# Performance work log

Hardware: AMD Instinct MI355X
Metric: run time of the kernel (lower is better)

The kernel has to match this reference:

```python
import jax, jax.numpy as jnp
import numpy as np

N_S = 4096      # number of sentences
N_K = 8192      # number of knowledge entries
HID = 1024      # settings.hidden_dim
SENT = 1024     # settings.sent_dim


def setup_inputs() -> dict:
    key = jax.random.key(0)
    ks = jax.random.split(key, 6)
    sentences = jax.random.normal(ks[0], (N_S, SENT), dtype=jnp.float32)
    knowledge = jax.random.normal(ks[1], (N_K, 3 * HID), dtype=jnp.float32)
    # Linear params stored as [in, out] for x @ W + b
    Ws = jax.random.normal(ks[2], (SENT, HID), dtype=jnp.float32) * 0.02
    bs = jnp.zeros((HID,), dtype=jnp.float32)
    Wk = jax.random.normal(ks[3], (3 * HID, HID), dtype=jnp.float32) * 0.02
    bk = jnp.zeros((HID,), dtype=jnp.float32)
    return {"sentences": sentences, "knowledge": knowledge,
            "Ws": Ws, "bs": bs, "Wk": Wk, "bk": bk}


def reference(sentences, knowledge, Ws, bs, Wk, bk):
    S = sentences @ Ws + bs                  # [N_s, h]
    K = knowledge @ Wk + bk                  # [N_k, h]
    align_scores = S @ K.T                   # [N_s, N_k]
    # NOTE: softmax over dim=0 (sentence axis), exactly as the torch module
    attentions = jax.nn.softmax(align_scores, axis=0)
    fused = attentions @ knowledge           # [N_s, 3h]
    return (fused, attentions)
```

## Files before the change

### kernel.cpp

```cpp
#include <hip/hip_runtime.h>
#include <hip/hip_bf16.h>
#include <cstdint>
#include <cstddef>

#define N_S 4096
#define N_Kn 8192
#define HID 1024
#define SENT 1024
#define K3 3072

typedef __attribute__((ext_vector_type(4))) float f4;
typedef __attribute__((ext_vector_type(8))) short bf8;
typedef __attribute__((ext_vector_type(4))) short bf4;
typedef unsigned short u16;

__device__ __forceinline__ u16 f2bf(float x) {
    __hip_bfloat16 h = __float2bfloat16(x);
    return __builtin_bit_cast(u16, h);
}
__device__ __forceinline__ float bf2f(u16 u) {
    union { unsigned int u; float f; } v; v.u = ((unsigned int)u) << 16;
    return v.f;
}

__device__ __forceinline__ void gl16(const u16* g, u16* l) {
    __builtin_amdgcn_global_load_lds(
        (const __attribute__((address_space(1))) void*)g,
        (__attribute__((address_space(3))) void*)l, 16, 0, 0);
}

__device__ __forceinline__ int xcd_swz(int bid, int nwg) {
    const int cpx = nwg >> 3;
    return (bid & 7) * cpx + (bid >> 3);
}

#define BARR __builtin_amdgcn_s_barrier()
#define PRIO1 __builtin_amdgcn_s_setprio(1)
#define PRIO0 __builtin_amdgcn_s_setprio(0)
#define VM7  asm volatile("s_waitcnt vmcnt(7)" ::: "memory")
#define VM6  asm volatile("s_waitcnt vmcnt(6)" ::: "memory")
#define VM0  asm volatile("s_waitcnt vmcnt(0)" ::: "memory")

__global__ __launch_bounds__(256) void transpose_split_f32(
    const float* __restrict__ in, u16* __restrict__ hi, u16* __restrict__ lo,
    int R, int C)
{
    __shared__ float tile[32][33];
    const int bx = blockIdx.x * 32, by = blockIdx.y * 32;
    const int tx = threadIdx.x & 31, ty = threadIdx.x >> 5;
#pragma unroll
    for (int i = 0; i < 32; i += 8)
        tile[ty + i][tx] = in[(size_t)(by + ty + i) * C + bx + tx];
    __syncthreads();
#pragma unroll
    for (int i = 0; i < 32; i += 8) {
        const float v = tile[tx][ty + i];
        const u16 h = f2bf(v);
        const size_t o = (size_t)(bx + ty + i) * R + by + tx;
        hi[o] = h;
        lo[o] = f2bf(v - bf2f(h));
    }
}

__global__ __launch_bounds__(256) void transpose_f32_bf16(
    const float* __restrict__ in, u16* __restrict__ out, int R, int C)
{
    __shared__ float tile[32][33];
    const int bx = blockIdx.x * 32, by = blockIdx.y * 32;
    const int tx = threadIdx.x & 31, ty = threadIdx.x >> 5;
#pragma unroll
    for (int i = 0; i < 32; i += 8)
        tile[ty + i][tx] = in[(size_t)(by + ty + i) * C + bx + tx];
    __syncthreads();
#pragma unroll
    for (int i = 0; i < 32; i += 8)
        out[(size_t)(bx + ty + i) * R + by + tx] = f2bf(tile[tx][ty + i]);
}

#define GB_LDA(buf, mh) \
  _Pragma("unroll") for (int mf_ = 0; mf_ < 2; ++mf_) \
  _Pragma("unroll") for (int kk_ = 0; kk_ < 2; ++kk_) \
    fa[mf_][kk_] = *(const bf8*)&sA[buf][(wm*64 + ((mh)*2+mf_)*16 + fr)*64 + (((kk_*4+kg) ^ (fr&7))<<3)];

#define GB_LDB(buf, nh, FB) \
  _Pragma("unroll") for (int nf_ = 0; nf_ < 3; ++nf_) \
  _Pragma("unroll") for (int kk_ = 0; kk_ < 2; ++kk_) \
    FB[nf_][kk_] = *(const bf8*)&sB[buf][(wn*96 + ((nh)*3+nf_)*16 + fr)*64 + (((kk_*4+kg) ^ (fr&7))<<3)];

#define GB_MMA(mh, nh, FB) \
  _Pragma("unroll") for (int kk_ = 0; kk_ < 2; ++kk_) \
  _Pragma("unroll") for (int mf_ = 0; mf_ < 2; ++mf_) \
  _Pragma("unroll") for (int nf_ = 0; nf_ < 3; ++nf_) \
    acc[(mh)*2+mf_][(nh)*3+nf_] = __builtin_amdgcn_mfma_f32_16x16x32_bf16( \
        fa[mf_][kk_], FB[nf_][kk_], acc[(mh)*2+mf_][(nh)*3+nf_], 0, 0, 0);

__global__ __launch_bounds__(512, 2) void gemm8b(
    const u16* __restrict__ A, const u16* __restrict__ B,
    float* __restrict__ C, int N, int Kd, int gx)
{
    __shared__ u16 sA[2][256 * 64];
    __shared__ u16 sB[2][192 * 64];

    const int swz = xcd_swz(blockIdx.x, gridDim.x);
    const int bx = swz % gx, by = swz / gx;
    const long brow = (long)by * 256, bcol = (long)bx * 192;

    const int t = threadIdx.x;
    const int w = t >> 6, l = t & 63;
    const int fr = l & 15, kg = l >> 4;
    const int wm = w >> 1;
    const int wn = w & 1;

    const int srow = t >> 3;
    const int schk = ((t & 7) ^ (srow & 7)) << 3;
    const int sldb = w << 9;

    const u16* pA0 = A + (brow +   0 + srow) * (long)Kd + schk;
    const u16* pA1 = A + (brow +  64 + srow) * (long)Kd + schk;
    const u16* pA2 = A + (brow + 128 + srow) * (long)Kd + schk;
    const u16* pA3 = A + (brow + 192 + srow) * (long)Kd + schk;
    const u16* pB0 = B + (bcol +   0 + srow) * (long)Kd + schk;
    const u16* pB1 = B + (bcol +  64 + srow) * (long)Kd + schk;
    const u16* pB2 = B + (bcol + 128 + srow) * (long)Kd + schk;

    auto stB3 = [&](int buf) {
        u16* base = &sB[buf][0];
        gl16(pB0, base + sldb);
        gl16(pB1, base + 4096 + sldb);
        gl16(pB2, base + 8192 + sldb);
    };
    auto stA4 = [&](int buf) {
        u16* base = &sA[buf][0];
        gl16(pA0, base + sldb);
        gl16(pA1, base + 4096 + sldb);
        gl16(pA2, base + 8192 + sldb);
        gl16(pA3, base + 12288 + sldb);
    };
    auto advance = [&]() {
        pA0 += 64; pA1 += 64; pA2 += 64; pA3 += 64;
        pB0 += 64; pB1 += 64; pB2 += 64;
    };

    f4 acc[4][6];
#pragma unroll
    for (int m = 0; m < 4; ++m)
#pragma unroll
        for (int n = 0; n < 6; ++n) acc[m][n] = (f4){0.f, 0.f, 0.f, 0.f};

    bf8 fa[2][2], fb0[3][2], fb1[3][2];

    const int NK = Kd >> 6;

    stB3(0); stA4(0); advance();
    stB3(1); stA4(1); advance();
    VM7;
    BARR;
    GB_LDB(0, 0, fb0);

    for (int kt = 0; kt < NK; ++kt) {
        const int buf = kt & 1;
        const bool s2 = kt + 2 < NK;
        const bool more = kt + 1 < NK;

        GB_LDA(buf, 0);
        BARR; PRIO1; GB_MMA(0, 0, fb0); PRIO0;

        GB_LDB(buf, 1, fb1);
        BARR; PRIO1; GB_MMA(0, 1, fb1); PRIO0;

        GB_LDA(buf, 1);
        if (s2) { stB3(buf); }
        BARR; PRIO1; GB_MMA(1, 0, fb0); PRIO0;

        if (s2) { stA4(buf); VM7; } else { VM0; }
        BARR;
        if (more) { GB_LDB(buf ^ 1, 0, fb0); }
        PRIO1; GB_MMA(1, 1, fb1); PRIO0;
        advance();
    }

#pragma unroll
    for (int n = 0; n < 6; ++n) {
        const long c = bcol + wn * 96 + n * 16 + fr;
#pragma unroll
        for (int m = 0; m < 4; ++m) {
            const long r0 = brow + wm * 64 + m * 16 + kg * 4;
#pragma unroll
            for (int r = 0; r < 4; ++r)
                C[(r0 + r) * (long)N + c] = acc[m][n][r];
        }
    }
}

#define GS_LD(buf) \
  _Pragma("unroll") for (int m_ = 0; m_ < 4; ++m_) { \
    fah[m_] = *(const bf8*)&sAh[buf][(wm*64 + m_*16 + fr)*32 + kq]; \
    fal[m_] = *(const bf8*)&sAl[buf][(wm*64 + m_*16 + fr)*32 + kq]; } \
  _Pragma("unroll") for (int j_ = 0; j_ < 4; ++j_) { \
    fbh[j_] = *(const bf8*)&sBh[buf][(wn*64 + j_*16 + fr)*32 + kq]; \
    fbl[j_] = *(const bf8*)&sBl[buf][(wn*64 + j_*16 + fr)*32 + kq]; }

#define GS_MMA(nlo) \
  _Pragma("unroll") for (int m_ = 0; m_ < 4; ++m_) \
  _Pragma("unroll") for (int j_ = 0; j_ < 2; ++j_) { \
    const int n_ = (nlo)*2 + j_; \
    acc[m_][n_] = __builtin_amdgcn_mfma_f32_16x16x32_bf16(fah[m_], fbh[n_], acc[m_][n_], 0, 0, 0); \
    acc[m_][n_] = __builtin_amdgcn_mfma_f32_16x16x32_bf16(fah[m_], fbl[n_], acc[m_][n_], 0, 0, 0); \
    acc[m_][n_] = __builtin_amdgcn_mfma_f32_16x16x32_bf16(fal[m_], fbh[n_], acc[m_][n_], 0, 0, 0); }

__global__ __launch_bounds__(512, 2) void gemm8s(
    const u16* __restrict__ Ah, const u16* __restrict__ Al,
    const u16* __restrict__ Bh, const u16* __restrict__ Bl,
    float* __restrict__ C, int N, int Kd)
{
    __shared__ u16 sAh[2][8192], sAl[2][8192];
    __shared__ u16 sBh[2][4096], sBl[2][4096];

    const int bid = blockIdx.x;
    const int q = bid >> 3;
    const int by = (bid & 7) * 2 + (q & 1);
    const int bx = q >> 1;
    const long brow = (long)by * 256, bcol = (long)bx * 128;

    const int t = threadIdx.x;
    const int w = t >> 6, l = t & 63;
    const int fr = l & 15, kg = l >> 4;
    const int wm = w >> 1;
    const int wn = w & 1;
    const int kq = (kg ^ ((fr >> 1) & 3)) << 3;

    const int srow = t >> 2;
    const int schk = ((t & 3) ^ ((t >> 3) & 3)) << 3;
    const int sldb = w << 9;

    const u16* pAh0 = Ah + (brow + srow) * (long)Kd + schk;
    const u16* pAh1 = Ah + (brow + 128 + srow) * (long)Kd + schk;
    const u16* pAl0 = Al + (brow + srow) * (long)Kd + schk;
    const u16* pAl1 = Al + (brow + 128 + srow) * (long)Kd + schk;
    const u16* pBh0 = Bh + (bcol + srow) * (long)Kd + schk;
    const u16* pBl0 = Bl + (bcol + srow) * (long)Kd + schk;

    auto stage6 = [&](int buf) {
        gl16(pBh0, &sBh[buf][sldb]);
        gl16(pBl0, &sBl[buf][sldb]);
        gl16(pAh0, &sAh[buf][sldb]);
        gl16(pAh1, &sAh[buf][4096 + sldb]);
        gl16(pAl0, &sAl[buf][sldb]);
        gl16(pAl1, &sAl[buf][4096 + sldb]);
    };
    auto advance = [&]() {
        pAh0 += 32; pAh1 += 32; pAl0 += 32; pAl1 += 32;
        pBh0 += 32; pBl0 += 32;
    };

    f4 acc[4][4];
#pragma unroll
    for (int m = 0; m < 4; ++m)
#pragma unroll
        for (int n = 0; n < 4; ++n) acc[m][n] = (f4){0.f, 0.f, 0.f, 0.f};

    bf8 fah[4], fal[4], fbh[4], fbl[4];

    const int NK = Kd >> 5;

    stage6(0); advance();
    stage6(1); advance();
    VM6;
    BARR;

    for (int kt = 0; kt < NK; ++kt) {
        const int buf = kt & 1;
        const bool s2 = kt + 2 < NK;

        GS_LD(buf);
        BARR; PRIO1; GS_MMA(0); PRIO0;

        if (s2) { stage6(buf); VM6; } else { VM0; }
        BARR;
        PRIO1; GS_MMA(1); PRIO0;
        advance();
    }

#pragma unroll
    for (int n = 0; n < 4; ++n) {
        const long c = bcol + wn * 64 + n * 16 + fr;
#pragma unroll
        for (int m = 0; m < 4; ++m) {
            const long r0 = brow + wm * 64 + m * 16 + kg * 4;
#pragma unroll
            for (int r = 0; r < 4; ++r)
                C[(r0 + r) * (long)N + c] = acc[m][n][r];
        }
    }
}

template <bool SPLIT, bool AF32, bool EPIS>
__global__ __launch_bounds__(256) void gemm_mfma(
    const void* __restrict__ Aany, const u16* __restrict__ Alo_,
    const u16* __restrict__ Bhi_, const u16* __restrict__ Blo_,
    float* __restrict__ Cf, u16* __restrict__ Chi, u16* __restrict__ Clo,
    const float* __restrict__ bias, int N, int Kd, int gx)
{
    constexpr int SA = AF32 ? 48 : 32;
    __shared__ u16 sAh[128 * SA];
    __shared__ u16 sAl[SPLIT ? 128 * SA : 8];
    __shared__ u16 sBh[128 * 32];
    __shared__ u16 sBl[SPLIT ? 128 * 32 : 8];

    const int swz = xcd_swz(blockIdx.x, gridDim.x);
    const int nst_x = gx >> 2;
    const int st = swz >> 4, off = swz & 15;
    const int bxi = (st % nst_x) * 4 + (off & 3);
    const int byi = (st / nst_x) * 4 + (off >> 2);

    const int t = threadIdx.x;
    const int w = t >> 6;
    const int l = t & 63;
    const long brow = (long)byi * 128;
    const long bcol = (long)bxi * 128;

    const int grow = l >> 2;
    const int gcol = ((l & 3) ^ ((l >> 3) & 3)) * 8;

    const int wr = (w >> 1) * 64;
    const int wc = (w & 1) * 64;
    const int fr = l & 15;
    const int kg = l >> 4;
    const int kq = (kg ^ ((fr >> 1) & 3)) * 8;

    f4 acc[4][4];
#pragma unroll
    for (int m = 0; m < 4; m++)
#pragma unroll
        for (int n = 0; n < 4; n++) acc[m][n] = (f4){0.f, 0.f, 0.f, 0.f};

    const int nkt = Kd >> 5;
    for (int kt = 0; kt < nkt; ++kt) {
        const int k0 = kt * 32;

#pragma unroll
        for (int i = 0; i < 2; ++i) {
            const long r = bcol + i * 64 + w * 16 + grow;
            const int lb = i * 2048 + w * 512;
            gl16(Bhi_ + r * Kd + k0 + gcol, sBh + lb);
            if constexpr (SPLIT) gl16(Blo_ + r * Kd + k0 + gcol, sBl + lb);
        }

        if constexpr (!AF32) {
            const u16* Ahi = (const u16*)Aany;
#pragma unroll
            for (int i = 0; i < 2; ++i) {
                const long r = brow + i * 64 + w * 16 + grow;
                const int lb = i * 2048 + w * 512;
                gl16(Ahi + r * Kd + k0 + gcol, sAh + lb);
                if constexpr (SPLIT) gl16(Alo_ + r * Kd + k0 + gcol, sAl + lb);
            }
        } else {
            const float* Af = (const float*)Aany;
            const int ar = w * 8 + (l >> 3);
            const int cF = (l & 7) * 4;
#pragma unroll
            for (int j = 0; j < 4; ++j) {
                const int r = j * 32 + ar;
                const f4 v = *(const f4*)(Af + (brow + r) * (long)Kd + k0 + cF);
                u16 h[4], lw[4];
#pragma unroll
                for (int q = 0; q < 4; ++q) {
                    h[q] = f2bf(v[q]);
                    if constexpr (SPLIT) lw[q] = f2bf(v[q] - bf2f(h[q]));
                }
                *(bf4*)&sAh[r * SA + cF] = *(bf4*)h;
                if constexpr (SPLIT) *(bf4*)&sAl[r * SA + cF] = *(bf4*)lw;
            }
        }
        __syncthreads();

        bf8 fah[4], fbh[4], fal[4], fbl[4];
#pragma unroll
        for (int m = 0; m < 4; ++m) {
            if constexpr (AF32) {
                fah[m] = *(bf8*)&sAh[(wr + m * 16 + fr) * SA + kg * 8];
                if constexpr (SPLIT) fal[m] = *(bf8*)&sAl[(wr + m * 16 + fr) * SA + kg * 8];
            } else {
                fah[m] = *(bf8*)&sAh[(wr + m * 16 + fr) * 32 + kq];
                if constexpr (SPLIT) fal[m] = *(bf8*)&sAl[(wr + m * 16 + fr) * 32 + kq];
            }
            fbh[m] = *(bf8*)&sBh[(wc + m * 16 + fr) * 32 + kq];
            if constexpr (SPLIT) fbl[m] = *(bf8*)&sBl[(wc + m * 16 + fr) * 32 + kq];
        }
#pragma unroll
        for (int m = 0; m < 4; ++m)
#pragma unroll
            for (int n = 0; n < 4; ++n) {
                acc[m][n] = __builtin_amdgcn_mfma_f32_16x16x32_bf16(fah[m], fbh[n], acc[m][n], 0, 0, 0);
                if constexpr (SPLIT) {
                    acc[m][n] = __builtin_amdgcn_mfma_f32_16x16x32_bf16(fah[m], fbl[n], acc[m][n], 0, 0, 0);
                    acc[m][n] = __builtin_amdgcn_mfma_f32_16x16x32_bf16(fal[m], fbh[n], acc[m][n], 0, 0, 0);
                }
            }
        __syncthreads();
    }

#pragma unroll
    for (int n = 0; n < 4; ++n) {
        const long c = bcol + wc + n * 16 + fr;
        float bv = 0.f;
        if constexpr (EPIS) bv = bias[c];
#pragma unroll
        for (int m = 0; m < 4; ++m) {
            const long r0 = brow + wr + m * 16 + kg * 4;
#pragma unroll
            for (int r = 0; r < 4; ++r) {
                const float v = acc[m][n][r] + bv;
                if constexpr (EPIS) {
                    const u16 h = f2bf(v);
                    Chi[(r0 + r) * (long)N + c] = h;
                    Clo[(r0 + r) * (long)N + c] = f2bf(v - bf2f(h));
                } else {
                    Cf[(r0 + r) * (long)N + c] = v;
                }
            }
        }
    }
}

#define RCHUNK 128

__global__ __launch_bounds__(256) void softmax_partial(
    const float* __restrict__ align, float* __restrict__ pm, float* __restrict__ ps)
{
    const int col = blockIdx.x * 256 + threadIdx.x;
    const int r0 = blockIdx.y * RCHUNK;
    float m = -3.4e38f;
    for (int r = 0; r < RCHUNK; r++)
        m = fmaxf(m, align[(size_t)(r0 + r) * N_Kn + col]);
    float s = 0.f;
    for (int r = 0; r < RCHUNK; r++)
        s += __expf(align[(size_t)(r0 + r) * N_Kn + col] - m);
    pm[(size_t)blockIdx.y * N_Kn + col] = m;
    ps[(size_t)blockIdx.y * N_Kn + col] = s;
}

__global__ __launch_bounds__(256) void softmax_combine(
    const float* __restrict__ pm, const float* __restrict__ ps,
    float* __restrict__ fm, float* __restrict__ fsinv)
{
    const int col = blockIdx.x * 256 + threadIdx.x;
    float m = -3.4e38f;
#pragma unroll
    for (int i = 0; i < 32; i++) m = fmaxf(m, pm[(size_t)i * N_Kn + col]);
    float s = 0.f;
#pragma unroll
    for (int i = 0; i < 32; i++)
        s += ps[(size_t)i * N_Kn + col] * __expf(pm[(size_t)i * N_Kn + col] - m);
    fm[col] = m;
    fsinv[col] = 1.f / s;
}

__global__ __launch_bounds__(256) void softmax_norm(
    float* __restrict__ align, u16* __restrict__ abf,
    const float* __restrict__ fm, const float* __restrict__ fsinv)
{
    const int col = blockIdx.x * 256 + threadIdx.x;
    const int r0 = blockIdx.y * RCHUNK;
    const float m = fm[col], si = fsinv[col];
    for (int r = 0; r < RCHUNK; r++) {
        const size_t idx = (size_t)(r0 + r) * N_Kn + col;
        const float v = __expf(align[idx] - m) * si;
        align[idx] = v;
        abf[idx] = f2bf(v);
    }
}

extern "C" void kernel_launch(void* const* d_in, const int* in_sizes, int n_in,
                              void* d_out, int out_size, void* d_ws, size_t ws_size,
                              hipStream_t stream)
{
    const float* sentences = (const float*)d_in[0];
    const float* knowledge = (const float*)d_in[1];
    const float* Ws = (const float*)d_in[2];
    const float* bs = (const float*)d_in[3];
    const float* Wk = (const float*)d_in[4];
    const float* bk = (const float*)d_in[5];

    float* out_fused = (float*)d_out;
    float* out_attn = (float*)d_out + (size_t)N_S * K3;

    char* w = (char*)d_ws;
    u16* attn_bf = (u16*)w;
    u16* WsT_hi = (u16*)w; w += (size_t)HID * SENT * 2;
    u16* WsT_lo = (u16*)w; w += (size_t)HID * SENT * 2;
    u16* WkT_hi = (u16*)w; w += (size_t)HID * K3 * 2;
    u16* WkT_lo = (u16*)w; w += (size_t)HID * K3 * 2;
    u16* S_hi   = (u16*)w; w += (size_t)N_S * HID * 2;
    u16* S_lo   = (u16*)w; w += (size_t)N_S * HID * 2;
    u16* K_hi   = (u16*)w; w += (size_t)N_Kn * HID * 2;
    u16* K_lo   = (u16*)w; w += (size_t)N_Kn * HID * 2;
    u16* kT     = (u16*)w; w += (size_t)K3 * N_Kn * 2;
    float* pm   = (float*)w; w += (size_t)32 * N_Kn * 4;
    float* ps   = (float*)w; w += (size_t)32 * N_Kn * 4;
    float* fm   = (float*)w; w += (size_t)N_Kn * 4;
    float* fsv  = (float*)w; w += (size_t)N_Kn * 4;

    transpose_split_f32<<<dim3(HID / 32, SENT / 32), 256, 0, stream>>>(Ws, WsT_hi, WsT_lo, SENT, HID);
    transpose_split_f32<<<dim3(HID / 32, K3 / 32), 256, 0, stream>>>(Wk, WkT_hi, WkT_lo, K3, HID);
    transpose_f32_bf16<<<dim3(K3 / 32, N_Kn / 32), 256, 0, stream>>>(knowledge, kT, N_Kn, K3);

    gemm_mfma<true, true, true><<<(HID / 128) * (N_S / 128), 256, 0, stream>>>(
        sentences, nullptr, WsT_hi, WsT_lo, nullptr, S_hi, S_lo, bs, HID, SENT, HID / 128);

    gemm_mfma<true, true, true><<<(HID / 128) * (N_Kn / 128), 256, 0, stream>>>(
        knowledge, nullptr, WkT_hi, WkT_lo, nullptr, K_hi, K_lo, bk, HID, K3, HID / 128);

    gemm8s<<<(N_Kn / 128) * (N_S / 256), 512, 0, stream>>>(
        S_hi, S_lo, K_hi, K_lo, out_attn, N_Kn, HID);

    softmax_partial<<<dim3(N_Kn / 256, N_S / RCHUNK), 256, 0, stream>>>(out_attn, pm, ps);
    softmax_combine<<<dim3(N_Kn / 256), 256, 0, stream>>>(pm, ps, fm, fsv);
    softmax_norm<<<dim3(N_Kn / 256, N_S / RCHUNK), 256, 0, stream>>>(out_attn, attn_bf, fm, fsv);

    gemm8b<<<(K3 / 192) * (N_S / 256), 512, 0, stream>>>(
        attn_bf, kT, out_fused, K3, N_Kn, K3 / 192);
}
```

Baseline: 753.2 us.

## Fuse column softmax partial max/sum into attention GEMM epilogue

Computes per-column max and sum-of-exp partials for each 256-row tile directly from the GEMM accumulators, reducing across lanes with shuffles and across waves through reused shared memory. The separate softmax_partial kernel is removed, along with its full re-read of the fp32 alignment matrix, and the combine step now merges 16 partials instead of 32. In exchange, the GEMM epilogue gains several block barriers and exp work.

```diff
diff --git a/kernel.cpp b/kernel.cpp
--- a/kernel.cpp
+++ b/kernel.cpp
@@ -211,7 +211,8 @@
 __global__ __launch_bounds__(512, 2) void gemm8s(
     const u16* __restrict__ Ah, const u16* __restrict__ Al,
     const u16* __restrict__ Bh, const u16* __restrict__ Bl,
-    float* __restrict__ C, int N, int Kd)
+    float* __restrict__ C, float* __restrict__ pm, float* __restrict__ ps,
+    int N, int Kd)
 {
     __shared__ u16 sAh[2][8192], sAl[2][8192];
     __shared__ u16 sBh[2][4096], sBl[2][4096];
@@ -292,6 +293,62 @@
                 C[(r0 + r) * (long)N + c] = acc[m][n][r];
         }
     }
+
+    float* red = (float*)&sAh[0][0];
+    float lmax[4];
+#pragma unroll
+    for (int n = 0; n < 4; ++n) {
+        float m = -3.4e38f;
+#pragma unroll
+        for (int mm = 0; mm < 4; ++mm)
+#pragma unroll
+            for (int r = 0; r < 4; ++r) m = fmaxf(m, acc[mm][n][r]);
+        m = fmaxf(m, __shfl_xor(m, 16, 64));
+        m = fmaxf(m, __shfl_xor(m, 32, 64));
+        lmax[n] = m;
+    }
+    BARR;
+    if (kg == 0) {
+#pragma unroll
+        for (int n = 0; n < 4; ++n)
+            red[wm * 128 + wn * 64 + n * 16 + fr] = lmax[n];
+    }
+    BARR;
+    float bmax[4];
+#pragma unroll
+    for (int n = 0; n < 4; ++n) {
+        const int c = wn * 64 + n * 16 + fr;
+        bmax[n] = fmaxf(fmaxf(red[c], red[128 + c]),
+                        fmaxf(red[256 + c], red[384 + c]));
+    }
+    BARR;
+    float lsum[4];
+#pragma unroll
+    for (int n = 0; n < 4; ++n) {
+        float s = 0.f;
+#pragma unroll
+        for (int mm = 0; mm < 4; ++mm)
+#pragma unroll
+            for (int r = 0; r < 4; ++r) s += __expf(acc[mm][n][r] - bmax[n]);
+        s += __shfl_xor(s, 16, 64);
+        s += __shfl_xor(s, 32, 64);
+        lsum[n] = s;
+    }
+    if (kg == 0) {
+#pragma unroll
+        for (int n = 0; n < 4; ++n)
+            red[wm * 128 + wn * 64 + n * 16 + fr] = lsum[n];
+    }
+    BARR;
+    if (wm == 0 && kg == 0) {
+#pragma unroll
+        for (int n = 0; n < 4; ++n) {
+            const int c = wn * 64 + n * 16 + fr;
+            const float bs = red[c] + red[128 + c] + red[256 + c] + red[384 + c];
+            pm[(size_t)by * N + bcol + c] = bmax[n];
+            ps[(size_t)by * N + bcol + c] = bs;
+        }
+    }
 }
 
 template <bool SPLIT, bool AF32, bool EPIS>
@@ -426,21 +483,6 @@
 
 #define RCHUNK 128
 
-__global__ __launch_bounds__(256) void softmax_partial(
-    const float* __restrict__ align, float* __restrict__ pm, float* __restrict__ ps)
-{
-    const int col = blockIdx.x * 256 + threadIdx.x;
-    const int r0 = blockIdx.y * RCHUNK;
-    float m = -3.4e38f;
-    for (int r = 0; r < RCHUNK; r++)
-        m = fmaxf(m, align[(size_t)(r0 + r) * N_Kn + col]);
-    float s = 0.f;
-    for (int r = 0; r < RCHUNK; r++)
-        s += __expf(align[(size_t)(r0 + r) * N_Kn + col] - m);
-    pm[(size_t)blockIdx.y * N_Kn + col] = m;
-    ps[(size_t)blockIdx.y * N_Kn + col] = s;
-}
-
 __global__ __launch_bounds__(256) void softmax_combine(
     const float* __restrict__ pm, const float* __restrict__ ps,
     float* __restrict__ fm, float* __restrict__ fsinv)
@@ -448,10 +490,10 @@
     const int col = blockIdx.x * 256 + threadIdx.x;
     float m = -3.4e38f;
 #pragma unroll
-    for (int i = 0; i < 32; i++) m = fmaxf(m, pm[(size_t)i * N_Kn + col]);
+    for (int i = 0; i < 16; i++) m = fmaxf(m, pm[(size_t)i * N_Kn + col]);
     float s = 0.f;
 #pragma unroll
-    for (int i = 0; i < 32; i++)
+    for (int i = 0; i < 16; i++)
         s += ps[(size_t)i * N_Kn + col] * __expf(pm[(size_t)i * N_Kn + col] - m);
     fm[col] = m;
     fsinv[col] = 1.f / s;
@@ -497,8 +539,8 @@
     u16* K_hi   = (u16*)w; w += (size_t)N_Kn * HID * 2;
     u16* K_lo   = (u16*)w; w += (size_t)N_Kn * HID * 2;
     u16* kT     = (u16*)w; w += (size_t)K3 * N_Kn * 2;
-    float* pm   = (float*)w; w += (size_t)32 * N_Kn * 4;
-    float* ps   = (float*)w; w += (size_t)32 * N_Kn * 4;
+    float* pm   = (float*)w; w += (size_t)16 * N_Kn * 4;
+    float* ps   = (float*)w; w += (size_t)16 * N_Kn * 4;
     float* fm   = (float*)w; w += (size_t)N_Kn * 4;
     float* fsv  = (float*)w; w += (size_t)N_Kn * 4;
 
@@ -513,9 +555,8 @@
         knowledge, nullptr, WkT_hi, WkT_lo, nullptr, K_hi, K_lo, bk, HID, K3, HID / 128);
 
     gemm8s<<<(N_Kn / 128) * (N_S / 256), 512, 0, stream>>>(
-        S_hi, S_lo, K_hi, K_lo, out_attn, N_Kn, HID);
-
-    softmax_partial<<<dim3(N_Kn / 256, N_S / RCHUNK), 256, 0, stream>>>(out_attn, pm, ps);
+        S_hi, S_lo, K_hi, K_lo, out_attn, pm, ps, N_Kn, HID);
+
     softmax_combine<<<dim3(N_Kn / 256), 256, 0, stream>>>(pm, ps, fm, fsv);
     softmax_norm<<<dim3(N_Kn / 256, N_S / RCHUNK), 256, 0, stream>>>(out_attn, attn_bf, fm, fsv);
 
```

After: 691.0 us. 1.09x faster.
